# Optimization experiments

Measured on AMD Instinct MI355X. Metric: run time of the kernel, lower is better.

The kernel has to match this reference:

```python
import jax, jax.numpy as jnp
import numpy as np

NEG = -1000000000.0

def setup_inputs() -> dict:
    key = jax.random.key(0)
    ks = jax.random.split(key, 6)
    B, V, F, H = 8, 4, 256, 768
    video_features = jax.random.normal(ks[0], (B, V, F, H), dtype=jnp.float32)
    video_attention_mask = jax.random.randint(ks[1], (B, V, F), 0, 2) > 0  # True = masked
    s = 1.0 / np.sqrt(H)
    Wqkv = jax.random.normal(ks[2], (3 * H, H), dtype=jnp.float32) * s
    bqkv = jax.random.normal(ks[3], (3 * H,), dtype=jnp.float32) * 0.01
    Wo = jax.random.normal(ks[4], (H, H), dtype=jnp.float32) * s
    bo = jax.random.normal(ks[5], (H,), dtype=jnp.float32) * 0.01
    return {"video_features": video_features, "video_attention_mask": video_attention_mask,
            "Wqkv": Wqkv, "bqkv": bqkv, "Wo": Wo, "bo": bo}

def reference(video_features, video_attention_mask, Wqkv, bqkv, Wo, bo):
    B, V, F, H = video_features.shape
    n_heads = 12
    head_dim = H // n_heads
    S = V * F  # total frames
    x = video_features.reshape(B, S, H)
    mask = video_attention_mask.reshape(B, S)
    # fused QKV projection (torch Linear: x @ W.T + b)
    qkv = x @ Wqkv.T + bqkv                      # [B, S, 3H]
    qkv = qkv.reshape(B, S, n_heads, 3 * head_dim).transpose(0, 2, 1, 3)  # [B, h, S, 3d]
    q, k, v = jnp.split(qkv, 3, axis=-1)         # each [B, h, S, d]
    scores = jnp.einsum('bhqd,bhkd->bhqk', q, k) / np.sqrt(head_dim)
    scores = jnp.where(mask[:, None, None, :], NEG, scores)
    attn = jax.nn.softmax(scores, axis=-1)       # dropout p=0 (eval) -> identity
    out = jnp.einsum('bhqk,bhkd->bhqd', attn, v) # [B, h, S, d]
    out = out.transpose(0, 2, 1, 3).reshape(B, S, H)
    out = out @ Wo.T + bo
    return out.reshape(B, V, F, H)
```

## Files before the change

kernel.cpp:

```cpp
#include <hip/hip_runtime.h>
#include <stdint.h>

typedef unsigned short u16;
typedef unsigned int u32;
typedef __attribute__((ext_vector_type(8))) unsigned short u16x8;
typedef __attribute__((ext_vector_type(4))) unsigned short u16x4;
typedef __attribute__((ext_vector_type(4))) float f32x4;
typedef __attribute__((ext_vector_type(16))) float f32x16;
typedef __attribute__((ext_vector_type(4))) float floatx4;
typedef __attribute__((ext_vector_type(8))) __bf16 bf16x8;


__device__ __forceinline__ u16 f2bf(float f) {
  union { float f; unsigned u; } c; c.f = f;
  unsigned r = c.u + 0x7fffu + ((c.u >> 16) & 1u);
  return (u16)(r >> 16);
}

__device__ __forceinline__ u32 packbf2(float lo, float hi) {
  return (u32)f2bf(lo) | ((u32)f2bf(hi) << 16);
}

__device__ __forceinline__ bf16x8 ld_bf8(const u16* p) {
  return __builtin_bit_cast(bf16x8, *(const u16x8*)p);
}

__device__ __forceinline__ float fexp2(float x) {
#if __has_builtin(__builtin_amdgcn_exp2f)
  return __builtin_amdgcn_exp2f(x);
#else
  float r; asm("v_exp_f32 %0, %1" : "=v"(r) : "v"(x)); return r;
#endif
}

__device__ __forceinline__ void glds16(const void* g, void* l) {
  __builtin_amdgcn_global_load_lds(
      (const __attribute__((address_space(1))) void*)g,
      (__attribute__((address_space(3))) void*)l, 16, 0, 0);
}

__global__ void convert_kernel(const float* __restrict__ x,
                               const float* __restrict__ w1,
                               const float* __restrict__ w2,
                               u16* __restrict__ xb,
                               u16* __restrict__ w1b,
                               u16* __restrict__ w2b) {
  const long NX = 6291456 / 4, NW1 = 1769472 / 4, NW2 = 589824 / 4;
  const long total = NX + NW1 + NW2;
  for (long i = (long)blockIdx.x * 256 + threadIdx.x; i < total;
       i += (long)gridDim.x * 256) {
    const float* src; u16* dst; long j;
    if (i < NX)            { src = x;  dst = xb;  j = i; }
    else if (i < NX + NW1) { src = w1; dst = w1b; j = i - NX; }
    else                   { src = w2; dst = w2b; j = i - NX - NW1; }
    floatx4 v = ((const floatx4*)src)[j];
    u16x4 o;
    o[0] = f2bf(v[0]); o[1] = f2bf(v[1]); o[2] = f2bf(v[2]); o[3] = f2bf(v[3]);
    ((u16x4*)dst)[j] = o;
  }
}

__global__ __launch_bounds__(256, 2)
void qkv_gemm(const u16* __restrict__ A, const u16* __restrict__ W,
              const float* __restrict__ bias,
              u16* __restrict__ qb, u16* __restrict__ kb, u16* __restrict__ vtb) {
  __shared__ __align__(16) u16 lds[30720];
  const int tid = threadIdx.x;
  const int lane = tid & 63, wid = tid >> 6;
  const int wm = wid >> 1, wn = wid & 1;
  const int l15 = lane & 15, l4 = lane >> 4;

  const int p = blockIdx.x;
  const int xcd = p & 7, i = p >> 3;
  const int by = xcd * 8 + i / 12;
  const int bx = i % 12;
  const int rowA0 = by * 128, rowB0 = bx * 192;

  const int rlo = lane >> 3;
  const u16* gA[2];
  const u16* gB[3];
#pragma unroll
  for (int c = 0; c < 2; ++c) {
    int mr = wid * 16 + c * 8 + rlo;
    int sl = (lane & 7) ^ (mr & 7);
    gA[c] = A + (size_t)(rowA0 + 2 * mr + (sl >> 2)) * 768 + (sl & 3) * 8;
  }
#pragma unroll
  for (int c = 0; c < 3; ++c) {
    int mr = wid * 24 + c * 8 + rlo;
    int sl = (lane & 7) ^ (mr & 7);
    gB[c] = W + (size_t)(rowB0 + 2 * mr + (sl >> 2)) * 768 + (sl & 3) * 8;
  }

  f32x4 acc[4][6];
  const f32x4 vz = {0.f, 0.f, 0.f, 0.f};
#pragma unroll
  for (int mi = 0; mi < 4; ++mi)
#pragma unroll
    for (int nj = 0; nj < 6; ++nj) acc[mi][nj] = vz;

#define QSTAGE(kb_, k0_)                                                   \
  {                                                                        \
    u16* bA_ = lds + (kb_) * 4096;                                         \
    u16* bB_ = lds + 12288 + (kb_) * 6144;                                 \
    _Pragma("unroll") for (int c = 0; c < 2; ++c)                          \
        glds16(gA[c] + (k0_), bA_ + (wid * 16 + c * 8) * 64);              \
    _Pragma("unroll") for (int c = 0; c < 3; ++c)                          \
        glds16(gB[c] + (k0_), bB_ + (wid * 24 + c * 8) * 64);              \
  }

  QSTAGE(0, 0);
  QSTAGE(1, 32);

  for (int ks = 0; ks < 24; ++ks) {
    const int cb = ks % 3;
    const u16* cA = lds + cb * 4096;
    const u16* cB = lds + 12288 + cb * 6144;

    __builtin_amdgcn_s_barrier();
    if (ks < 22) {
      QSTAGE((ks + 2) % 3, (ks + 2) * 32);
      asm volatile("s_waitcnt vmcnt(10)" ::: "memory");
    } else if (ks == 22) {
      asm volatile("s_waitcnt vmcnt(5)" ::: "memory");
    } else {
      asm volatile("s_waitcnt vmcnt(0)" ::: "memory");
    }
    __builtin_amdgcn_s_barrier();
    __builtin_amdgcn_sched_barrier(0);

    bf16x8 af[4], bfr[6];
#pragma unroll
    for (int mi = 0; mi < 4; ++mi) {
      int m = wm * 64 + mi * 16 + l15;
      int mr = m >> 1;
      int sp = ((m & 1) * 4 + l4) ^ (mr & 7);
      af[mi] = ld_bf8(cA + mr * 64 + sp * 8);
    }
#pragma unroll
    for (int nj = 0; nj < 6; ++nj) {
      int n = wn * 96 + nj * 16 + l15;
      int mr = n >> 1;
      int sp = ((n & 1) * 4 + l4) ^ (mr & 7);
      bfr[nj] = ld_bf8(cB + mr * 64 + sp * 8);
    }
    __builtin_amdgcn_s_setprio(1);
#pragma unroll
    for (int mi = 0; mi < 4; ++mi)
#pragma unroll
      for (int nj = 0; nj < 6; ++nj)
        acc[mi][nj] = __builtin_amdgcn_mfma_f32_16x16x32_bf16(
            af[mi], bfr[nj], acc[mi][nj], 0, 0, 0);
    __builtin_amdgcn_s_setprio(0);
  }
#undef QSTAGE

  const float QSC = 0.125f * 1.44269504088896f;
  const int batch = by >> 3, s0 = (by & 7) * 128;
  const size_t gbase = (size_t)(batch * 12 + bx) * 65536;

  float bias_v[6];
#pragma unroll
  for (int nj = 0; nj < 6; ++nj)
    bias_v[nj] = bias[rowB0 + wn * 96 + nj * 16 + l15];

  __syncthreads();

#pragma unroll
  for (int nj = 0; nj < 6; ++nj) {
    int col0 = wn * 96 + nj * 16;
    int band = col0 >> 6;
    int dd = (col0 & 63) + l15;
    float bv = bias_v[nj];
    if (band < 2) {
      float sc = (band == 0) ? QSC : 1.0f;
      u16* reg = lds + band * 9216;
#pragma unroll
      for (int mi = 0; mi < 4; ++mi)
#pragma unroll
        for (int r = 0; r < 4; ++r) {
          int m = wm * 64 + mi * 16 + l4 * 4 + r;
          reg[m * 72 + dd] = f2bf((acc[mi][nj][r] + bv) * sc);
        }
    } else {
      u16* reg = lds + 18432;
#pragma unroll
      for (int mi = 0; mi < 4; ++mi)
#pragma unroll
        for (int r = 0; r < 4; r += 2) {
          int m = wm * 64 + mi * 16 + l4 * 4 + r;
          *(u32*)&reg[dd * 136 + m] =
              packbf2(acc[mi][nj][r] + bv, acc[mi][nj][r + 1] + bv);
        }
    }
  }
  __syncthreads();

#pragma unroll
  for (int j = 0; j < 4; ++j) {
    int c = tid + j * 256;
    int m = c >> 3, dd0 = (c & 7) << 3;
    u16x8 v = *(const u16x8*)&lds[m * 72 + dd0];
    *(u16x8*)&qb[gbase + (size_t)(s0 + m) * 64 + dd0] = v;
  }
#pragma unroll
  for (int j = 0; j < 4; ++j) {
    int c = tid + j * 256;
    int m = c >> 3, dd0 = (c & 7) << 3;
    u16x8 v = *(const u16x8*)&lds[9216 + m * 72 + dd0];
    *(u16x8*)&kb[gbase + (size_t)(s0 + m) * 64 + dd0] = v;
  }
#pragma unroll
  for (int j = 0; j < 4; ++j) {
    int c = tid + j * 256;
    int dd = c >> 4, m0 = (c & 15) << 3;
    u16x8 v = *(const u16x8*)&lds[18432 + dd * 136 + m0];
    *(u16x8*)&vtb[gbase + (size_t)dd * 1024 + s0 + m0] = v;
  }
}

__global__ __launch_bounds__(256, 3)
void attn_kernel(const u16* __restrict__ qb, const u16* __restrict__ kb,
                 const u16* __restrict__ vtb, const void* __restrict__ maskp,
                 u16* __restrict__ x2) {
  const int bh = blockIdx.x, qt = blockIdx.y;
  const int b = bh / 12, h = bh - b * 12;
  const int tid = threadIdx.x;
  const int w = tid >> 6, lane = tid & 63;
  const int l31 = lane & 31, hi = lane >> 5;

  __shared__ float mbias[1024];
  __shared__ int any_big;
  __shared__ __align__(16) u16 plds[4][32][40];
  __shared__ __align__(16) u16 kvs[16384];

  if (tid == 0) any_big = 0;
  __syncthreads();
  {
    const unsigned* mu = (const unsigned*)maskp;
    int loc = 0;
    for (int i = tid; i < 2048; i += 256)
      if (mu[i] > 1u) loc = 1;
    if (loc) atomicOr(&any_big, 1);
  }
  __syncthreads();
  const float CEXP = 23.0831206542234f;
  if (any_big) {
    const unsigned char* mb = (const unsigned char*)maskp;
    for (int i = tid; i < 1024; i += 256)
      mbias[i] = mb[b * 1024 + i] ? -100000.0f : -CEXP;
  } else {
    const int* mi_ = (const int*)maskp;
    for (int i = tid; i < 1024; i += 256)
      mbias[i] = mi_[b * 1024 + i] ? -100000.0f : -CEXP;
  }

  const size_t base = (size_t)bh * 65536;
  const int q0w = qt * 128 + w * 32;

  const int rlo = lane >> 3;
  const int cg = (lane & 7) ^ (rlo & 7);
  const int srow = w * 8 + rlo;
  const u16* kg0 = kb + base + (size_t)srow * 64 + cg * 8;
  const u16* vg0 = vtb + base + (size_t)srow * 1024 + cg * 8;
  u16* kd0 = kvs + w * 512;
  u16* vd0 = kvs + 4096 + w * 512;

  bf16x8 qf[4];
#pragma unroll
  for (int dstep = 0; dstep < 4; ++dstep)
    qf[dstep] = ld_bf8(qb + base + (size_t)(q0w + l31) * 64 + dstep * 16 + hi * 8);

  f32x16 o[2];
#pragma unroll
  for (int dh = 0; dh < 2; ++dh)
#pragma unroll
    for (int r = 0; r < 16; ++r) o[dh][r] = 0.f;
  float ps = 0.f;

  glds16(kg0, kd0);
  glds16(kg0 + 32 * 64, kd0 + 2048);
  glds16(vg0, vd0);
  glds16(vg0 + 32 * 1024, vd0 + 2048);
  __syncthreads();

  for (int kt = 0; kt < 16; ++kt) {
    const int cur = kt & 1;
    if (kt < 15) {
      const int nxt = cur ^ 1;
      glds16(kg0 + (kt + 1) * 4096, kd0 + nxt * 8192);
      glds16(kg0 + (kt + 1) * 4096 + 32 * 64, kd0 + nxt * 8192 + 2048);
      glds16(vg0 + (kt + 1) * 64, vd0 + nxt * 8192);
      glds16(vg0 + (kt + 1) * 64 + 32 * 1024, vd0 + nxt * 8192 + 2048);
    }

    const u16* Kl = kvs + cur * 8192;
    const u16* Vl = kvs + cur * 8192 + 4096;

#pragma unroll
    for (int kk = 0; kk < 2; ++kk) {
      f32x16 s;
#pragma unroll
      for (int r = 0; r < 16; ++r) s[r] = 0.f;
      const int rk = kk * 32 + l31;
      __builtin_amdgcn_s_setprio(1);
#pragma unroll
      for (int dstep = 0; dstep < 4; ++dstep) {
        bf16x8 kf = ld_bf8(Kl + rk * 64 + ((dstep * 2 + hi) ^ (rk & 7)) * 8);
        s = __builtin_amdgcn_mfma_f32_32x32x16_bf16(kf, qf[dstep], s, 0, 0, 0);
      }
      __builtin_amdgcn_s_setprio(0);
#pragma unroll
      for (int g = 0; g < 4; ++g) {
        f32x4 bv = *(const f32x4*)(mbias + kt * 64 + kk * 32 + g * 8 + hi * 4);
        float p0 = fexp2(s[g * 4 + 0] + bv[0]);
        float p1 = fexp2(s[g * 4 + 1] + bv[1]);
        float p2 = fexp2(s[g * 4 + 2] + bv[2]);
        float p3 = fexp2(s[g * 4 + 3] + bv[3]);
        ps += (p0 + p1) + (p2 + p3);
        const int colb = g * 8 + hi * 4;
        *(u32*)&plds[w][l31][colb]     = packbf2(p0, p1);
        *(u32*)&plds[w][l31][colb + 2] = packbf2(p2, p3);
      }

      __builtin_amdgcn_s_setprio(1);
#pragma unroll
      for (int t = 0; t < 2; ++t) {
        bf16x8 pf = ld_bf8(&plds[w][l31][t * 16 + hi * 8]);
#pragma unroll
        for (int dh = 0; dh < 2; ++dh) {
          const int rv = dh * 32 + l31;
          const int gv = kk * 4 + t * 2 + hi;
          bf16x8 vf = ld_bf8(Vl + rv * 64 + (gv ^ (rv & 7)) * 8);
          o[dh] = __builtin_amdgcn_mfma_f32_32x32x16_bf16(vf, pf, o[dh], 0, 0, 0);
        }
      }
      __builtin_amdgcn_s_setprio(0);
    }

    __syncthreads();
  }

  ps += __shfl_xor(ps, 32, 64);
  float inv = 1.0f / ps;

  u16* obuf = kvs + w * 2304;
#pragma unroll
  for (int dh = 0; dh < 2; ++dh)
#pragma unroll
    for (int j = 0; j < 8; ++j) {
      u32 v = packbf2(o[dh][2 * j] * inv, o[dh][2 * j + 1] * inv);
      int col = dh * 32 + 8 * (j >> 1) + 4 * hi + 2 * (j & 1);
      *(u32*)(obuf + l31 * 72 + col) = v;
    }

  {
    int row2 = lane >> 1, ch = lane & 1;
    const u16* srcp = obuf + row2 * 72 + ch * 32;
    u16x8 t0 = *(const u16x8*)(srcp);
    u16x8 t1 = *(const u16x8*)(srcp + 8);
    u16x8 t2 = *(const u16x8*)(srcp + 16);
    u16x8 t3 = *(const u16x8*)(srcp + 24);
    size_t m = (size_t)b * 1024 + qt * 128 + w * 32 + row2;
    u16* dst = x2 + m * 768 + h * 64 + ch * 32;
    *(u16x8*)dst = t0;
    *(u16x8*)(dst + 8) = t1;
    *(u16x8*)(dst + 16) = t2;
    *(u16x8*)(dst + 24) = t3;
  }
}

__global__ __launch_bounds__(256, 2)
void out_gemm(const u16* __restrict__ A, const u16* __restrict__ W,
              const float* __restrict__ bias, float* __restrict__ out) {
  __shared__ __align__(16) u16 lA[2][128 * 64];
  __shared__ __align__(16) u16 lB[2][128 * 64];
  const int tid = threadIdx.x;
  const int lane = tid & 63, wid = tid >> 6;
  const int wm = wid >> 1, wn = wid & 1;
  const int l15 = lane & 15, l4 = lane >> 4;
  const int h7 = l15 & 7;

  const int p = blockIdx.x;
  const int xcd = p & 7, i = p >> 3;
  const int by = xcd * 8 + i / 6;
  const int bx = i % 6;
  const int rowA0 = by * 128, rowB0 = bx * 128;

  const int rlo = lane >> 3;
  const int swz = (lane & 7) ^ rlo;
  const u16* ga = A + (size_t)(rowA0 + wid * 8 + rlo) * 768 + swz * 8;
  const u16* gb = W + (size_t)(rowB0 + wid * 8 + rlo) * 768 + swz * 8;

  f32x4 acc[4][4];
  const f32x4 vz = {0.f, 0.f, 0.f, 0.f};
#pragma unroll
  for (int ii = 0; ii < 4; ++ii)
#pragma unroll
    for (int j = 0; j < 4; ++j) acc[ii][j] = vz;

#define OSTAGE(buf, k0)                                          \
  {                                                              \
    _Pragma("unroll") for (int j = 0; j < 4; ++j) {              \
      glds16(ga + (k0) + j * 32 * 768, lA[buf] + j * 2048 + wid * 512); \
      glds16(gb + (k0) + j * 32 * 768, lB[buf] + j * 2048 + wid * 512); \
    }                                                            \
  }

  OSTAGE(0, 0);

  for (int ks = 0; ks < 12; ++ks) {
    const int cur = ks & 1;
    __builtin_amdgcn_s_barrier();
    if (ks < 11) {
      OSTAGE(cur ^ 1, (ks + 1) * 64);
      asm volatile("s_waitcnt vmcnt(8)" ::: "memory");
    } else {
      asm volatile("s_waitcnt vmcnt(0)" ::: "memory");
    }
    __builtin_amdgcn_s_barrier();
    __builtin_amdgcn_sched_barrier(0);

    bf16x8 af[4][2], bfr[4][2];
#pragma unroll
    for (int mi = 0; mi < 4; ++mi)
#pragma unroll
      for (int kk = 0; kk < 2; ++kk)
        af[mi][kk] = ld_bf8(lA[cur] + (wm * 64 + mi * 16 + l15) * 64 +
                            (((kk * 4 + l4) ^ h7) * 8));
#pragma unroll
    for (int ni = 0; ni < 4; ++ni)
#pragma unroll
      for (int kk = 0; kk < 2; ++kk)
        bfr[ni][kk] = ld_bf8(lB[cur] + (wn * 64 + ni * 16 + l15) * 64 +
                             (((kk * 4 + l4) ^ h7) * 8));
    __builtin_amdgcn_s_setprio(1);
#pragma unroll
    for (int mi = 0; mi < 4; ++mi)
#pragma unroll
      for (int ni = 0; ni < 4; ++ni)
#pragma unroll
        for (int kk = 0; kk < 2; ++kk)
          acc[mi][ni] = __builtin_amdgcn_mfma_f32_16x16x32_bf16(
              af[mi][kk], bfr[ni][kk], acc[mi][ni], 0, 0, 0);
    __builtin_amdgcn_s_setprio(0);
  }
#undef OSTAGE

#pragma unroll
  for (int ni = 0; ni < 4; ++ni) {
    int n = rowB0 + wn * 64 + ni * 16 + l15;
    float bn_ = bias[n];
#pragma unroll
    for (int mi = 0; mi < 4; ++mi)
#pragma unroll
      for (int r = 0; r < 4; ++r) {
        int m = rowA0 + wm * 64 + mi * 16 + l4 * 4 + r;
        out[(size_t)m * 768 + n] = acc[mi][ni][r] + bn_;
      }
  }
}

extern "C" void kernel_launch(void* const* d_in, const int* in_sizes, int n_in,
                              void* d_out, int out_size, void* d_ws, size_t ws_size,
                              hipStream_t stream) {
  const float* x    = (const float*)d_in[0];
  const void*  mask = d_in[1];
  const float* wqkv = (const float*)d_in[2];
  const float* bqkv = (const float*)d_in[3];
  const float* wo   = (const float*)d_in[4];
  const float* bo   = (const float*)d_in[5];
  float* out = (float*)d_out;

  u16* ws = (u16*)d_ws;
  u16* xbf   = ws;
  u16* wqkvb = ws + 6291456;
  u16* wob   = ws + 8060928;
  u16* qbuf  = ws + 8650752;
  u16* kbuf  = ws + 14942208;
  u16* vtbuf = ws + 21233664;
  u16* x2buf = ws + 27525120;

  convert_kernel<<<2048, 256, 0, stream>>>(x, wqkv, wo, xbf, wqkvb, wob);
  qkv_gemm<<<768, 256, 0, stream>>>(xbf, wqkvb, bqkv, qbuf, kbuf, vtbuf);
  attn_kernel<<<dim3(96, 8), 256, 0, stream>>>(qbuf, kbuf, vtbuf, mask, x2buf);
  out_gemm<<<384, 256, 0, stream>>>(x2buf, wob, bo, out);
}
```

Before: 114.5 us.

## Batch QK MFMAs per tile, swizzle P scratch, use hardware bf16 pack

The attention inner loop now issues the QK^T MFMAs for both 32-key halves of a tile up front, instead of interleaving them with the softmax/PV work. This gives the scheduler more independent matrix work to overlap with the exp and LDS traffic. The per-warp P scratch buffer gets an XOR swizzle on column groups to cut LDS bank conflicts. Software bf16 rounding is replaced by the v_cvt_pk_bf16_f32 instruction. The cost is higher register pressure from two live score accumulators, which could hurt occupancy under launch_bounds(256,3).

Measured after the change: 114.4 us. Within noise of the previous version (-0.1%).

```diff
diff --git a/kernel.cpp b/kernel.cpp
--- a/kernel.cpp
+++ b/kernel.cpp
@@ -19,6 +19,12 @@
 
 __device__ __forceinline__ u32 packbf2(float lo, float hi) {
   return (u32)f2bf(lo) | ((u32)f2bf(hi) << 16);
+}
+
+__device__ __forceinline__ u32 cvtpk(float lo, float hi) {
+  u32 r;
+  asm("v_cvt_pk_bf16_f32 %0, %1, %2" : "=v"(r) : "v"(lo), "v"(hi));
+  return r;
 }
 
 __device__ __forceinline__ bf16x8 ld_bf8(const u16* p) {
@@ -228,6 +234,8 @@
   const int tid = threadIdx.x;
   const int w = tid >> 6, lane = tid & 63;
   const int l31 = lane & 31, hi = lane >> 5;
+  const int xr = (l31 >> 3) & 3;
+  const int l7 = l31 & 7;
 
   __shared__ float mbias[1024];
   __shared__ int any_big;
@@ -297,36 +305,41 @@
     const u16* Kl = kvs + cur * 8192;
     const u16* Vl = kvs + cur * 8192 + 4096;
 
+    f32x16 sarr[2];
+#pragma unroll
+    for (int r = 0; r < 16; ++r) { sarr[0][r] = 0.f; sarr[1][r] = 0.f; }
+    __builtin_amdgcn_s_setprio(1);
+#pragma unroll
+    for (int dstep = 0; dstep < 4; ++dstep) {
+      bf16x8 kf = ld_bf8(Kl + l31 * 64 + ((dstep * 2 + hi) ^ l7) * 8);
+      sarr[0] = __builtin_amdgcn_mfma_f32_32x32x16_bf16(kf, qf[dstep], sarr[0], 0, 0, 0);
+    }
+#pragma unroll
+    for (int dstep = 0; dstep < 4; ++dstep) {
+      bf16x8 kf = ld_bf8(Kl + (32 + l31) * 64 + ((dstep * 2 + hi) ^ l7) * 8);
+      sarr[1] = __builtin_amdgcn_mfma_f32_32x32x16_bf16(kf, qf[dstep], sarr[1], 0, 0, 0);
+    }
+    __builtin_amdgcn_s_setprio(0);
+
 #pragma unroll
     for (int kk = 0; kk < 2; ++kk) {
-      f32x16 s;
-#pragma unroll
-      for (int r = 0; r < 16; ++r) s[r] = 0.f;
-      const int rk = kk * 32 + l31;
-      __builtin_amdgcn_s_setprio(1);
-#pragma unroll
-      for (int dstep = 0; dstep < 4; ++dstep) {
-        bf16x8 kf = ld_bf8(Kl + rk * 64 + ((dstep * 2 + hi) ^ (rk & 7)) * 8);
-        s = __builtin_amdgcn_mfma_f32_32x32x16_bf16(kf, qf[dstep], s, 0, 0, 0);
-      }
-      __builtin_amdgcn_s_setprio(0);
 #pragma unroll
       for (int g = 0; g < 4; ++g) {
         f32x4 bv = *(const f32x4*)(mbias + kt * 64 + kk * 32 + g * 8 + hi * 4);
-        float p0 = fexp2(s[g * 4 + 0] + bv[0]);
-        float p1 = fexp2(s[g * 4 + 1] + bv[1]);
-        float p2 = fexp2(s[g * 4 + 2] + bv[2]);
-        float p3 = fexp2(s[g * 4 + 3] + bv[3]);
+        float p0 = fexp2(sarr[kk][g * 4 + 0] + bv[0]);
+        float p1 = fexp2(sarr[kk][g * 4 + 1] + bv[1]);
+        float p2 = fexp2(sarr[kk][g * 4 + 2] + bv[2]);
+        float p3 = fexp2(sarr[kk][g * 4 + 3] + bv[3]);
         ps += (p0 + p1) + (p2 + p3);
-        const int colb = g * 8 + hi * 4;
-        *(u32*)&plds[w][l31][colb]     = packbf2(p0, p1);
-        *(u32*)&plds[w][l31][colb + 2] = packbf2(p2, p3);
+        const int pb = ((g ^ xr) * 8) + hi * 4;
+        *(u32*)&plds[w][l31][pb]     = cvtpk(p0, p1);
+        *(u32*)&plds[w][l31][pb + 2] = cvtpk(p2, p3);
       }
 
       __builtin_amdgcn_s_setprio(1);
 #pragma unroll
       for (int t = 0; t < 2; ++t) {
-        bf16x8 pf = ld_bf8(&plds[w][l31][t * 16 + hi * 8]);
+        bf16x8 pf = ld_bf8(&plds[w][l31][(((t * 2 + hi) ^ xr) * 8)]);
 #pragma unroll
         for (int dh = 0; dh < 2; ++dh) {
           const int rv = dh * 32 + l31;
@@ -349,7 +362,7 @@
   for (int dh = 0; dh < 2; ++dh)
 #pragma unroll
     for (int j = 0; j < 8; ++j) {
-      u32 v = packbf2(o[dh][2 * j] * inv, o[dh][2 * j + 1] * inv);
+      u32 v = cvtpk(o[dh][2 * j] * inv, o[dh][2 * j + 1] * inv);
       int col = dh * 32 + 8 * (j >> 1) + 4 * hi + 2 * (j & 1);
       *(u32*)(obuf + l31 * 72 + col) = v;
     }
```

## Load K/V fragments directly from global into registers, dropping LDS staging

Applied to the files above, without the earlier changes.

The attention kernel no longer stages K and V tiles through shared memory with global_load_lds double buffering and per-tile barriers. Each wave now loads its K and V MFMA fragments straight from global memory into registers, prefetching the next K tile while the current one is consumed. Softmax probabilities and the output are packed to bf16 with the hardware v_cvt_pk_bf16_f32 instruction instead of manual rounding. The occupancy hint drops from 3 to 2 blocks per CU to leave room for the extra fragment registers. In exchange, K/V loads are repeated across the four waves and rely on L2/L1 instead of being shared through LDS.

Result: slower. 161.6 us (+41.1%).

```diff
diff --git a/kernel.cpp b/kernel.cpp
--- a/kernel.cpp
+++ b/kernel.cpp
@@ -5,6 +5,7 @@
 typedef unsigned int u32;
 typedef __attribute__((ext_vector_type(8))) unsigned short u16x8;
 typedef __attribute__((ext_vector_type(4))) unsigned short u16x4;
+typedef __attribute__((ext_vector_type(2))) unsigned int u32x2;
 typedef __attribute__((ext_vector_type(4))) float f32x4;
 typedef __attribute__((ext_vector_type(16))) float f32x16;
 typedef __attribute__((ext_vector_type(4))) float floatx4;
@@ -19,6 +20,12 @@
 
 __device__ __forceinline__ u32 packbf2(float lo, float hi) {
   return (u32)f2bf(lo) | ((u32)f2bf(hi) << 16);
+}
+
+__device__ __forceinline__ u32 cvtpk(float lo, float hi) {
+  u32 r;
+  asm("v_cvt_pk_bf16_f32 %0, %1, %2" : "=v"(r) : "v"(lo), "v"(hi));
+  return r;
 }
 
 __device__ __forceinline__ bf16x8 ld_bf8(const u16* p) {
@@ -219,7 +226,7 @@
   }
 }
 
-__global__ __launch_bounds__(256, 3)
+__global__ __launch_bounds__(256, 2)
 void attn_kernel(const u16* __restrict__ qb, const u16* __restrict__ kb,
                  const u16* __restrict__ vtb, const void* __restrict__ maskp,
                  u16* __restrict__ x2) {
@@ -232,7 +239,7 @@
   __shared__ float mbias[1024];
   __shared__ int any_big;
   __shared__ __align__(16) u16 plds[4][32][40];
-  __shared__ __align__(16) u16 kvs[16384];
+  __shared__ __align__(16) u16 obuf[4][32][72];
 
   if (tid == 0) any_big = 0;
   __syncthreads();
@@ -254,22 +261,17 @@
     for (int i = tid; i < 1024; i += 256)
       mbias[i] = mi_[b * 1024 + i] ? -100000.0f : -CEXP;
   }
+  __syncthreads();
 
   const size_t base = (size_t)bh * 65536;
   const int q0w = qt * 128 + w * 32;
-
-  const int rlo = lane >> 3;
-  const int cg = (lane & 7) ^ (rlo & 7);
-  const int srow = w * 8 + rlo;
-  const u16* kg0 = kb + base + (size_t)srow * 64 + cg * 8;
-  const u16* vg0 = vtb + base + (size_t)srow * 1024 + cg * 8;
-  u16* kd0 = kvs + w * 512;
-  u16* vd0 = kvs + 4096 + w * 512;
+  const u16* Kb = kb + base;
+  const u16* Vb = vtb + base;
 
   bf16x8 qf[4];
 #pragma unroll
-  for (int dstep = 0; dstep < 4; ++dstep)
-    qf[dstep] = ld_bf8(qb + base + (size_t)(q0w + l31) * 64 + dstep * 16 + hi * 8);
+  for (int ds = 0; ds < 4; ++ds)
+    qf[ds] = ld_bf8(qb + base + (size_t)(q0w + l31) * 64 + ds * 16 + hi * 8);
 
   f32x16 o[2];
 #pragma unroll
@@ -278,85 +280,90 @@
     for (int r = 0; r < 16; ++r) o[dh][r] = 0.f;
   float ps = 0.f;
 
-  glds16(kg0, kd0);
-  glds16(kg0 + 32 * 64, kd0 + 2048);
-  glds16(vg0, vd0);
-  glds16(vg0 + 32 * 1024, vd0 + 2048);
-  __syncthreads();
-
-  for (int kt = 0; kt < 16; ++kt) {
-    const int cur = kt & 1;
-    if (kt < 15) {
-      const int nxt = cur ^ 1;
-      glds16(kg0 + (kt + 1) * 4096, kd0 + nxt * 8192);
-      glds16(kg0 + (kt + 1) * 4096 + 32 * 64, kd0 + nxt * 8192 + 2048);
-      glds16(vg0 + (kt + 1) * 64, vd0 + nxt * 8192);
-      glds16(vg0 + (kt + 1) * 64 + 32 * 1024, vd0 + nxt * 8192 + 2048);
-    }
-
-    const u16* Kl = kvs + cur * 8192;
-    const u16* Vl = kvs + cur * 8192 + 4096;
-
-#pragma unroll
-    for (int kk = 0; kk < 2; ++kk) {
-      f32x16 s;
-#pragma unroll
-      for (int r = 0; r < 16; ++r) s[r] = 0.f;
-      const int rk = kk * 32 + l31;
-      __builtin_amdgcn_s_setprio(1);
-#pragma unroll
-      for (int dstep = 0; dstep < 4; ++dstep) {
-        bf16x8 kf = ld_bf8(Kl + rk * 64 + ((dstep * 2 + hi) ^ (rk & 7)) * 8);
-        s = __builtin_amdgcn_mfma_f32_32x32x16_bf16(kf, qf[dstep], s, 0, 0, 0);
-      }
-      __builtin_amdgcn_s_setprio(0);
-#pragma unroll
-      for (int g = 0; g < 4; ++g) {
-        f32x4 bv = *(const f32x4*)(mbias + kt * 64 + kk * 32 + g * 8 + hi * 4);
-        float p0 = fexp2(s[g * 4 + 0] + bv[0]);
-        float p1 = fexp2(s[g * 4 + 1] + bv[1]);
-        float p2 = fexp2(s[g * 4 + 2] + bv[2]);
-        float p3 = fexp2(s[g * 4 + 3] + bv[3]);
-        ps += (p0 + p1) + (p2 + p3);
-        const int colb = g * 8 + hi * 4;
-        *(u32*)&plds[w][l31][colb]     = packbf2(p0, p1);
-        *(u32*)&plds[w][l31][colb + 2] = packbf2(p2, p3);
-      }
-
-      __builtin_amdgcn_s_setprio(1);
-#pragma unroll
-      for (int t = 0; t < 2; ++t) {
-        bf16x8 pf = ld_bf8(&plds[w][l31][t * 16 + hi * 8]);
-#pragma unroll
-        for (int dh = 0; dh < 2; ++dh) {
-          const int rv = dh * 32 + l31;
-          const int gv = kk * 4 + t * 2 + hi;
-          bf16x8 vf = ld_bf8(Vl + rv * 64 + (gv ^ (rv & 7)) * 8);
-          o[dh] = __builtin_amdgcn_mfma_f32_32x32x16_bf16(vf, pf, o[dh], 0, 0, 0);
-        }
-      }
-      __builtin_amdgcn_s_setprio(0);
-    }
-
-    __syncthreads();
-  }
+  bf16x8 kfA[2][4], kfB[2][4], vf[2][2][2];
+
+#define KLOAD(DST, KT)                                                       \
+  _Pragma("unroll") for (int kk = 0; kk < 2; ++kk)                           \
+  _Pragma("unroll") for (int ds = 0; ds < 4; ++ds)                           \
+    DST[kk][ds] = ld_bf8(Kb + (size_t)((KT) * 64 + kk * 32 + l31) * 64 +     \
+                         ds * 16 + hi * 8);
+
+#define VLOAD(KT)                                                            \
+  _Pragma("unroll") for (int kk = 0; kk < 2; ++kk)                           \
+  _Pragma("unroll") for (int t = 0; t < 2; ++t)                              \
+  _Pragma("unroll") for (int dh = 0; dh < 2; ++dh)                           \
+    vf[kk][t][dh] = ld_bf8(Vb + (size_t)(dh * 32 + l31) * 1024 +             \
+                           (KT) * 64 + kk * 32 + t * 16 + hi * 8);
+
+#define SMPV(SV, KK, KT)                                                     \
+  {                                                                          \
+    _Pragma("unroll") for (int g = 0; g < 4; ++g) {                          \
+      f32x4 bv = *(const f32x4*)(mbias + (KT) * 64 + (KK) * 32 + g * 8 +     \
+                                 hi * 4);                                    \
+      float p0 = fexp2(SV[g * 4 + 0] + bv[0]);                               \
+      float p1 = fexp2(SV[g * 4 + 1] + bv[1]);                               \
+      float p2 = fexp2(SV[g * 4 + 2] + bv[2]);                               \
+      float p3 = fexp2(SV[g * 4 + 3] + bv[3]);                               \
+      ps += (p0 + p1) + (p2 + p3);                                           \
+      u32x2 pw; pw[0] = cvtpk(p0, p1); pw[1] = cvtpk(p2, p3);                \
+      *(u32x2*)&plds[w][l31][g * 8 + hi * 4] = pw;                           \
+    }                                                                        \
+    __builtin_amdgcn_s_setprio(1);                                           \
+    _Pragma("unroll") for (int t = 0; t < 2; ++t) {                          \
+      bf16x8 pf = ld_bf8(&plds[w][l31][t * 16 + hi * 8]);                    \
+      _Pragma("unroll") for (int dh = 0; dh < 2; ++dh)                       \
+        o[dh] = __builtin_amdgcn_mfma_f32_32x32x16_bf16(vf[KK][t][dh], pf,   \
+                                                        o[dh], 0, 0, 0);     \
+    }                                                                        \
+    __builtin_amdgcn_s_setprio(0);                                           \
+  }
+
+#define ASTEP(CUR, NXT, KT)                                                  \
+  {                                                                          \
+    VLOAD(KT);                                                               \
+    f32x16 s0, s1;                                                           \
+    _Pragma("unroll") for (int r = 0; r < 16; ++r) {                         \
+      s0[r] = 0.f; s1[r] = 0.f;                                              \
+    }                                                                        \
+    __builtin_amdgcn_s_setprio(1);                                           \
+    _Pragma("unroll") for (int ds = 0; ds < 4; ++ds)                         \
+      s0 = __builtin_amdgcn_mfma_f32_32x32x16_bf16(CUR[0][ds], qf[ds], s0,   \
+                                                   0, 0, 0);                 \
+    _Pragma("unroll") for (int ds = 0; ds < 4; ++ds)                         \
+      s1 = __builtin_amdgcn_mfma_f32_32x32x16_bf16(CUR[1][ds], qf[ds], s1,   \
+                                                   0, 0, 0);                 \
+    __builtin_amdgcn_s_setprio(0);                                           \
+    KLOAD(NXT, (KT) + 1);   \
+    SMPV(s0, 0, KT);                                                         \
+    SMPV(s1, 1, KT);                                                         \
+  }
+
+  KLOAD(kfA, 0);
+
+  for (int kt = 0; kt < 16; kt += 2) {
+    ASTEP(kfA, kfB, kt);
+    ASTEP(kfB, kfA, kt + 1);
+  }
+#undef ASTEP
+#undef SMPV
+#undef VLOAD
+#undef KLOAD
 
   ps += __shfl_xor(ps, 32, 64);
   float inv = 1.0f / ps;
 
-  u16* obuf = kvs + w * 2304;
 #pragma unroll
   for (int dh = 0; dh < 2; ++dh)
 #pragma unroll
     for (int j = 0; j < 8; ++j) {
-      u32 v = packbf2(o[dh][2 * j] * inv, o[dh][2 * j + 1] * inv);
+      u32 v = cvtpk(o[dh][2 * j] * inv, o[dh][2 * j + 1] * inv);
       int col = dh * 32 + 8 * (j >> 1) + 4 * hi + 2 * (j & 1);
-      *(u32*)(obuf + l31 * 72 + col) = v;
+      *(u32*)&obuf[w][l31][col] = v;
     }
 
   {
     int row2 = lane >> 1, ch = lane & 1;
-    const u16* srcp = obuf + row2 * 72 + ch * 32;
+    const u16* srcp = &obuf[w][row2][ch * 32];
     u16x8 t0 = *(const u16x8*)(srcp);
     u16x8 t1 = *(const u16x8*)(srcp + 8);
     u16x8 t2 = *(const u16x8*)(srcp + 16);
```

## Retile output GEMM to 128x192 with triple-buffered K=32 stages; use hardware bf16 pack

Applied to the files above, without the earlier changes.

The output projection GEMM moves from 128x128 tiles with K=64 double buffering to 128x192 tiles with K=32 stages and a three-buffer pipeline that keeps two loads in flight. A new LDS layout packs two rows per 64-element line with an XOR swizzle. The grid shrinks from 384 to 256 blocks, which raises per-block reuse of A and fits exactly one wave of blocks. Separately, the software bf16 rounding in the attention kernel is replaced with the v_cvt_pk_bf16_f32 instruction, which cuts ALU work in the softmax inner loop. The risks are more accumulator registers (24 tiles per wave) and fewer blocks for latency hiding.

After: 115.8 us. Within noise of the previous version (+1.1%).

```diff
diff --git a/kernel.cpp b/kernel.cpp
--- a/kernel.cpp
+++ b/kernel.cpp
@@ -5,6 +5,7 @@
 typedef unsigned int u32;
 typedef __attribute__((ext_vector_type(8))) unsigned short u16x8;
 typedef __attribute__((ext_vector_type(4))) unsigned short u16x4;
+typedef __attribute__((ext_vector_type(2))) unsigned int u32x2;
 typedef __attribute__((ext_vector_type(4))) float f32x4;
 typedef __attribute__((ext_vector_type(16))) float f32x16;
 typedef __attribute__((ext_vector_type(4))) float floatx4;
@@ -19,6 +20,12 @@
 
 __device__ __forceinline__ u32 packbf2(float lo, float hi) {
   return (u32)f2bf(lo) | ((u32)f2bf(hi) << 16);
+}
+
+__device__ __forceinline__ u32 cvtpk(float lo, float hi) {
+  u32 r;
+  asm("v_cvt_pk_bf16_f32 %0, %1, %2" : "=v"(r) : "v"(lo), "v"(hi));
+  return r;
 }
 
 __device__ __forceinline__ bf16x8 ld_bf8(const u16* p) {
@@ -319,8 +326,8 @@
         float p3 = fexp2(s[g * 4 + 3] + bv[3]);
         ps += (p0 + p1) + (p2 + p3);
         const int colb = g * 8 + hi * 4;
-        *(u32*)&plds[w][l31][colb]     = packbf2(p0, p1);
-        *(u32*)&plds[w][l31][colb + 2] = packbf2(p2, p3);
+        *(u32*)&plds[w][l31][colb]     = cvtpk(p0, p1);
+        *(u32*)&plds[w][l31][colb + 2] = cvtpk(p2, p3);
       }
 
       __builtin_amdgcn_s_setprio(1);
@@ -349,7 +356,7 @@
   for (int dh = 0; dh < 2; ++dh)
 #pragma unroll
     for (int j = 0; j < 8; ++j) {
-      u32 v = packbf2(o[dh][2 * j] * inv, o[dh][2 * j + 1] * inv);
+      u32 v = cvtpk(o[dh][2 * j] * inv, o[dh][2 * j + 1] * inv);
       int col = dh * 32 + 8 * (j >> 1) + 4 * hi + 2 * (j & 1);
       *(u32*)(obuf + l31 * 72 + col) = v;
     }
@@ -373,90 +380,107 @@
 __global__ __launch_bounds__(256, 2)
 void out_gemm(const u16* __restrict__ A, const u16* __restrict__ W,
               const float* __restrict__ bias, float* __restrict__ out) {
-  __shared__ __align__(16) u16 lA[2][128 * 64];
-  __shared__ __align__(16) u16 lB[2][128 * 64];
+  __shared__ __align__(16) u16 lds[30720];
   const int tid = threadIdx.x;
   const int lane = tid & 63, wid = tid >> 6;
   const int wm = wid >> 1, wn = wid & 1;
   const int l15 = lane & 15, l4 = lane >> 4;
-  const int h7 = l15 & 7;
 
   const int p = blockIdx.x;
   const int xcd = p & 7, i = p >> 3;
-  const int by = xcd * 8 + i / 6;
-  const int bx = i % 6;
-  const int rowA0 = by * 128, rowB0 = bx * 128;
+  const int by = xcd * 8 + i / 4;
+  const int bx = i % 4;
+  const int rowA0 = by * 128, rowB0 = bx * 192;
 
   const int rlo = lane >> 3;
-  const int swz = (lane & 7) ^ rlo;
-  const u16* ga = A + (size_t)(rowA0 + wid * 8 + rlo) * 768 + swz * 8;
-  const u16* gb = W + (size_t)(rowB0 + wid * 8 + rlo) * 768 + swz * 8;
-
-  f32x4 acc[4][4];
+  const u16* gA[2];
+  const u16* gB[3];
+#pragma unroll
+  for (int c = 0; c < 2; ++c) {
+    int mr = wid * 16 + c * 8 + rlo;
+    int sl = (lane & 7) ^ (mr & 7);
+    gA[c] = A + (size_t)(rowA0 + 2 * mr + (sl >> 2)) * 768 + (sl & 3) * 8;
+  }
+#pragma unroll
+  for (int c = 0; c < 3; ++c) {
+    int mr = wid * 24 + c * 8 + rlo;
+    int sl = (lane & 7) ^ (mr & 7);
+    gB[c] = W + (size_t)(rowB0 + 2 * mr + (sl >> 2)) * 768 + (sl & 3) * 8;
+  }
+
+  f32x4 acc[4][6];
   const f32x4 vz = {0.f, 0.f, 0.f, 0.f};
 #pragma unroll
-  for (int ii = 0; ii < 4; ++ii)
-#pragma unroll
-    for (int j = 0; j < 4; ++j) acc[ii][j] = vz;
-
-#define OSTAGE(buf, k0)                                          \
-  {                                                              \
-    _Pragma("unroll") for (int j = 0; j < 4; ++j) {              \
-      glds16(ga + (k0) + j * 32 * 768, lA[buf] + j * 2048 + wid * 512); \
-      glds16(gb + (k0) + j * 32 * 768, lB[buf] + j * 2048 + wid * 512); \
-    }                                                            \
+  for (int mi = 0; mi < 4; ++mi)
+#pragma unroll
+    for (int nj = 0; nj < 6; ++nj) acc[mi][nj] = vz;
+
+#define OSTAGE(kb_, k0_)                                                   \
+  {                                                                        \
+    u16* bA_ = lds + (kb_) * 4096;                                         \
+    u16* bB_ = lds + 12288 + (kb_) * 6144;                                 \
+    _Pragma("unroll") for (int c = 0; c < 2; ++c)                          \
+        glds16(gA[c] + (k0_), bA_ + (wid * 16 + c * 8) * 64);              \
+    _Pragma("unroll") for (int c = 0; c < 3; ++c)                          \
+        glds16(gB[c] + (k0_), bB_ + (wid * 24 + c * 8) * 64);              \
   }
 
   OSTAGE(0, 0);
-
-  for (int ks = 0; ks < 12; ++ks) {
-    const int cur = ks & 1;
+  OSTAGE(1, 32);
+
+  for (int ks = 0; ks < 24; ++ks) {
+    const int cb = ks % 3;
+    const u16* cA = lds + cb * 4096;
+    const u16* cB = lds + 12288 + cb * 6144;
+
     __builtin_amdgcn_s_barrier();
-    if (ks < 11) {
-      OSTAGE(cur ^ 1, (ks + 1) * 64);
-      asm volatile("s_waitcnt vmcnt(8)" ::: "memory");
+    if (ks < 22) {
+      OSTAGE((ks + 2) % 3, (ks + 2) * 32);
+      asm volatile("s_waitcnt vmcnt(10)" ::: "memory");
+    } else if (ks == 22) {
+      asm volatile("s_waitcnt vmcnt(5)" ::: "memory");
     } else {
       asm volatile("s_waitcnt vmcnt(0)" ::: "memory");
     }
     __builtin_amdgcn_s_barrier();
     __builtin_amdgcn_sched_barrier(0);
 
-    bf16x8 af[4][2], bfr[4][2];
+    bf16x8 af[4], bfr[6];
+#pragma unroll
+    for (int mi = 0; mi < 4; ++mi) {
+      int m = wm * 64 + mi * 16 + l15;
+      int mr = m >> 1;
+      int sp = ((m & 1) * 4 + l4) ^ (mr & 7);
+      af[mi] = ld_bf8(cA + mr * 64 + sp * 8);
+    }
+#pragma unroll
+    for (int nj = 0; nj < 6; ++nj) {
+      int n = wn * 96 + nj * 16 + l15;
+      int mr = n >> 1;
+      int sp = ((n & 1) * 4 + l4) ^ (mr & 7);
+      bfr[nj] = ld_bf8(cB + mr * 64 + sp * 8);
+    }
+    __builtin_amdgcn_s_setprio(1);
 #pragma unroll
     for (int mi = 0; mi < 4; ++mi)
 #pragma unroll
-      for (int kk = 0; kk < 2; ++kk)
-        af[mi][kk] = ld_bf8(lA[cur] + (wm * 64 + mi * 16 + l15) * 64 +
-                            (((kk * 4 + l4) ^ h7) * 8));
-#pragma unroll
-    for (int ni = 0; ni < 4; ++ni)
-#pragma unroll
-      for (int kk = 0; kk < 2; ++kk)
-        bfr[ni][kk] = ld_bf8(lB[cur] + (wn * 64 + ni * 16 + l15) * 64 +
-                             (((kk * 4 + l4) ^ h7) * 8));
-    __builtin_amdgcn_s_setprio(1);
-#pragma unroll
-    for (int mi = 0; mi < 4; ++mi)
-#pragma unroll
-      for (int ni = 0; ni < 4; ++ni)
-#pragma unroll
-        for (int kk = 0; kk < 2; ++kk)
-          acc[mi][ni] = __builtin_amdgcn_mfma_f32_16x16x32_bf16(
-              af[mi][kk], bfr[ni][kk], acc[mi][ni], 0, 0, 0);
+      for (int nj = 0; nj < 6; ++nj)
+        acc[mi][nj] = __builtin_amdgcn_mfma_f32_16x16x32_bf16(
+            af[mi], bfr[nj], acc[mi][nj], 0, 0, 0);
     __builtin_amdgcn_s_setprio(0);
   }
 #undef OSTAGE
 
 #pragma unroll
-  for (int ni = 0; ni < 4; ++ni) {
-    int n = rowB0 + wn * 64 + ni * 16 + l15;
+  for (int nj = 0; nj < 6; ++nj) {
+    int n = rowB0 + wn * 96 + nj * 16 + l15;
     float bn_ = bias[n];
 #pragma unroll
     for (int mi = 0; mi < 4; ++mi)
 #pragma unroll
       for (int r = 0; r < 4; ++r) {
         int m = rowA0 + wm * 64 + mi * 16 + l4 * 4 + r;
-        out[(size_t)m * 768 + n] = acc[mi][ni][r] + bn_;
+        out[(size_t)m * 768 + n] = acc[mi][nj][r] + bn_;
       }
   }
 }
@@ -484,5 +508,5 @@
   convert_kernel<<<2048, 256, 0, stream>>>(x, wqkv, wo, xbf, wqkvb, wob);
   qkv_gemm<<<768, 256, 0, stream>>>(xbf, wqkvb, bqkv, qbuf, kbuf, vtbuf);
   attn_kernel<<<dim3(96, 8), 256, 0, stream>>>(qbuf, kbuf, vtbuf, mask, x2buf);
-  out_gemm<<<384, 256, 0, stream>>>(x2buf, wob, bo, out);
-}
+  out_gemm<<<256, 256, 0, stream>>>(x2buf, wob, bo, out);
+}
```
